# Optimization experiments

Hardware: AMD Instinct MI355X
Metric: run time of the kernel (lower is better)

Reference implementation:

```python
import jax, jax.numpy as jnp
import numpy as np

H = 4            # attention heads
D_SUB = 32       # per-head hidden dim
D_HID = H * D_SUB
B = 100          # graphs in batch
N_PER = 5000     # nodes per graph
N = B * N_PER
DEG = 16         # avg degree
E = N * DEG
K_PER = 2500     # ceil(0.5 * N_PER), pooling_rate=0.5


def setup_inputs() -> dict:
    key = jax.random.key(0)
    k0, k1, k2, k3 = jax.random.split(key, 4)
    x = jax.random.normal(k0, (N, D_HID), jnp.float32)
    sub_xs = jax.random.normal(k1, (H, N, D_SUB), jnp.float32)
    # edges strictly within each graph (contiguous node blocks per graph)
    rng = np.random.default_rng(0)
    src = rng.integers(0, N_PER, size=(B, N_PER * DEG))
    dst = rng.integers(0, N_PER, size=(B, N_PER * DEG))
    off = (np.arange(B) * N_PER)[:, None]
    edge_index = jnp.asarray(
        np.stack([(src + off).reshape(-1), (dst + off).reshape(-1)]), jnp.int32)
    batch = jnp.repeat(jnp.arange(B, dtype=jnp.int32), N_PER)
    att_W = jax.random.normal(k2, (H, D_SUB, 1), jnp.float32) * 0.1
    att_b = jnp.zeros((H, 1), jnp.float32)
    score_W = jax.random.normal(k3, (1, 1), jnp.float32)
    score_b = jnp.zeros((1,), jnp.float32)
    return {"x": x, "sub_xs": sub_xs, "att_W": att_W, "att_b": att_b,
            "score_W": score_W, "score_b": score_b,
            "edge_index": edge_index, "batch": batch}


def _gcn_prop(h, row, col, dis):
    # PyG GCNConv propagation with self-loops: D^{-1/2}(A+I)D^{-1/2} h
    norm = (dis[row] * dis[col])[:, None]                       # [E,1]
    agg = jax.ops.segment_sum(h[row] * norm, col, num_segments=N)
    return agg + h * (dis ** 2)[:, None]                        # self-loop term deg^-1


def reference(x, sub_xs, att_W, att_b, score_W, score_b, edge_index, batch):
    row, col = edge_index[0], edge_index[1]
    deg = 1.0 + jax.ops.segment_sum(jnp.ones((E,), x.dtype), col, num_segments=N)
    dis = deg ** -0.5
    # per-head GCNConv(sub_hidden, 1): [H,N,1]
    h = jnp.einsum('hnd,hdo->hno', sub_xs, att_W)
    agg = jax.vmap(lambda hh: _gcn_prop(hh, row, col, dis))(h) + att_b[:, None, :]
    # torch F.softmax with implicit dim=1 on [N,1] -> softmax over size-1 axis (all ones); faithful
    att = jax.nn.softmax(agg, axis=-1)                          # [H,N,1]
    pool = att.mean(axis=0)                                     # 'mean' att pooling -> [N,1]
    # pooling_score_layer = GCNConv(1,1)
    score = (_gcn_prop(pool @ score_W, row, col, dis) + score_b)[:, 0]  # [N]
    # batched topk: equal-size contiguous graphs -> static k per graph
    _, idx = jax.lax.top_k(score.reshape(B, N_PER), K_PER)      # sorted desc per graph
    perm = (idx + (jnp.arange(B) * N_PER)[:, None]).reshape(-1) # [B*K_PER]
    x_new = x[perm] * jnp.tanh(score[perm])[:, None]            # global att weighting
    batch_new = batch[perm]
    # filter_adj: keep edges with both endpoints selected, reindex to new ids
    n_idx = jnp.full((N,), -1, jnp.int32).at[perm].set(
        jnp.arange(B * K_PER, dtype=jnp.int32))
    r, c = n_idx[row], n_idx[col]
    keep = (r >= 0) & (c >= 0)
    pos = jnp.nonzero(keep, size=E, fill_value=0)[0]            # compacted, order-preserving
    valid = jnp.arange(E) < keep.sum()
    edge_new = jnp.stack([jnp.where(valid, r[pos], -1),
                          jnp.where(valid, c[pos], -1)])        # [2,E], -1 padded
    return x_new, edge_new, batch_new, perm
```

## Files before the change

### kernel.cpp

```cpp
#include <hip/hip_runtime.h>
#include <hip/hip_bf16.h>

constexpr int H      = 4;
constexpr int D_SUB  = 32;
constexpr int D_HID  = 128;
constexpr int B      = 100;
constexpr int N_PER  = 5000;
constexpr int N      = B * N_PER;
constexpr int DEG    = 16;
constexpr int E      = N * DEG;
constexpr int E_PER  = N_PER * DEG;
constexpr int K_PER  = 2500;
constexpr int NK     = B * K_PER;

constexpr int EPB    = 4096;
constexpr int EPT    = 16;
constexpr int NBLK_E = (E + EPB - 1) / EPB;

constexpr int SUBR   = 625;
constexpr int LCAP   = 11640;

constexpr int M      = 8192;

constexpr unsigned long long FLG_A = 1ull << 62;
constexpr unsigned long long FLG_I = 2ull << 62;

__device__ __forceinline__ int swz8(int bid, int chunk) {
    return (bid & 7) * chunk + (bid >> 3);
}

__device__ __forceinline__ int ph(int i) { return i + (i >> 3); }

__global__ __launch_bounds__(1024) void k_count(const int* __restrict__ col,
                                                int* __restrict__ cnt2) {
    __shared__ int h[N_PER];
    int lb = swz8(blockIdx.x, 25);
    int g = lb >> 1, half = lb & 1;
    for (int i = threadIdx.x; i < N_PER; i += 1024) h[i] = 0;
    __syncthreads();
    int ebase = g * E_PER + half * (E_PER / 2);
    int nbase = g * N_PER;
    const int4* c4 = (const int4*)(col + ebase);
    for (int i = threadIdx.x; i < E_PER / 2 / 4; i += 1024) {
        int4 v = c4[i];
        atomicAdd(&h[v.x - nbase], 1);
        atomicAdd(&h[v.y - nbase], 1);
        atomicAdd(&h[v.z - nbase], 1);
        atomicAdd(&h[v.w - nbase], 1);
    }
    __syncthreads();
    int* dst = cnt2 + half * N + nbase;
    for (int i = threadIdx.x; i < N_PER; i += 1024) dst[i] = h[i];
}

__global__ void k_dis(const int* __restrict__ cnt2, int* __restrict__ cnt,
                      float* __restrict__ dis) {
    int v = blockIdx.x * blockDim.x + threadIdx.x;
    if (v < N) {
        int c = cnt2[v] + cnt2[N + v];
        cnt[v] = c;
        float d = (float)(1 + c);
        dis[v] = __fdiv_rn(1.0f, __fsqrt_rn(d));
    }
}

__global__ __launch_bounds__(1024) void k_score_fused(const int* __restrict__ row,
                                                      const int* __restrict__ col,
                                                      const int* __restrict__ cnt,
                                                      const float* __restrict__ dis,
                                                      const float* __restrict__ scW,
                                                      const float* __restrict__ scB,
                                                      float* __restrict__ score) {
    __shared__ float dis_l[N_PER];
    __shared__ int   wsum[16];
    __shared__ int   offs_l[SUBR];
    __shared__ int   curs_l[SUBR];
    __shared__ int   list[LCAP];
    int lb = swz8(blockIdx.x, 100);
    int g = lb >> 3, q = lb & 7;
    int t = threadIdx.x;
    int nbase = g * N_PER;
    int ebase = g * E_PER;
    int lo = q * SUBR;

    const float4* d4 = (const float4*)(dis + nbase);
    for (int j4 = t; j4 < N_PER / 4; j4 += 1024) {
        float4 dv4 = d4[j4];
        int j = 4 * j4;
        dis_l[j]     = dv4.x;
        dis_l[j + 1] = dv4.y;
        dis_l[j + 2] = dv4.z;
        dis_l[j + 3] = dv4.w;
    }

    int v = (t < SUBR) ? cnt[nbase + lo + t] : 0;
    int lane = t & 63, wid = t >> 6;
    int x = v;
#pragma unroll
    for (int s = 1; s < 64; s <<= 1) {
        int o = __shfl_up(x, s, 64);
        if (lane >= s) x += o;
    }
    if (lane == 63) wsum[wid] = x;
    __syncthreads();
    if (wid == 0) {
        int ws = (lane < 16) ? wsum[lane] : 0;
#pragma unroll
        for (int s = 1; s < 16; s <<= 1) {
            int o = __shfl_up(ws, s, 64);
            if (lane >= s) ws += o;
        }
        if (lane < 16) wsum[lane] = ws;
    }
    __syncthreads();
    int incl = x + (wid > 0 ? wsum[wid - 1] : 0);
    if (t < SUBR) { offs_l[t] = incl - v + t; curs_l[t] = 0; }
    __syncthreads();

    const int4* c4 = (const int4*)(col + ebase);
    const int4* r4 = (const int4*)(row + ebase);
    for (int i4 = t; i4 < E_PER / 4; i4 += 1024) {
        int4 cv = c4[i4];
        int4 rv = r4[i4];
        int i0 = 4 * i4;
#pragma unroll
        for (int m = 0; m < 4; m++) {
            int cl = ((m == 0) ? cv.x : (m == 1) ? cv.y : (m == 2) ? cv.z : cv.w) - nbase;
            int rl = ((m == 0) ? rv.x : (m == 1) ? rv.y : (m == 2) ? rv.z : rv.w) - nbase;
            unsigned d = (unsigned)(cl - lo);
            if (d < (unsigned)SUBR) {
                int i = i0 + m;
                int slot = atomicAdd(&curs_l[d], 1);
                int pos = offs_l[d] + slot;
                if (pos < LCAP) list[pos] = (i << 13) | rl;
            }
        }
    }
    __syncthreads();

    if (t < SUBR) {
        int base = offs_l[t];
        int k = v;
        if (base + k > LCAP) k = 0;
        for (int i = 1; i < k; i++) {
            int key = list[base + i];
            int j = i - 1;
            while (j >= 0 && list[base + j] > key) { list[base + j + 1] = list[base + j]; j--; }
            list[base + j + 1] = key;
        }
        float w = scW[0];
        float dv = dis_l[lo + t];
        float s = 0.0f;
        for (int i = 0; i < k; i++) {
            int rl = list[base + i] & 8191;
            s = __fadd_rn(s, __fmul_rn(w, __fmul_rn(dis_l[rl], dv)));
        }
        s = __fadd_rn(s, __fmul_rn(w, __fmul_rn(dv, dv)));
        s = __fadd_rn(s, scB[0]);
        score[nbase + lo + t] = s;
    }
}

__global__ __launch_bounds__(1024) void k_topk(const float* __restrict__ score,
                                               float* __restrict__ out_batch,
                                               float* __restrict__ out_perm,
                                               int* __restrict__ perm_i,
                                               int* __restrict__ n_idx) {
    __shared__ unsigned long long keys[M + (M >> 3)];
    int b = blockIdx.x, t = threadIdx.x;
    int base = 8 * t;

    unsigned long long v[8];
    if (t < 625) {
        const float4* s4 = (const float4*)(score + b * N_PER + base);
        float4 f0 = s4[0], f1 = s4[1];
        float fs[8] = {f0.x, f0.y, f0.z, f0.w, f1.x, f1.y, f1.z, f1.w};
#pragma unroll
        for (int m = 0; m < 8; m++) {
            unsigned u = __float_as_uint(fs[m]);
            unsigned asc = u ^ ((u & 0x80000000u) ? 0xFFFFFFFFu : 0x80000000u);
            v[m] = ((unsigned long long)(~asc) << 32) | (unsigned)(base + m);
        }
    } else {
#pragma unroll
        for (int m = 0; m < 8; m++) v[m] = ~0ull;
    }

#define CEV(x, y, up) { if ((v[x] > v[y]) == (up)) { unsigned long long tmp = v[x]; v[x] = v[y]; v[y] = tmp; } }
    CEV(0, 1, true)  CEV(2, 3, false) CEV(4, 5, true)  CEV(6, 7, false)
    CEV(0, 2, true)  CEV(1, 3, true)  CEV(4, 6, false) CEV(5, 7, false)
    CEV(0, 1, true)  CEV(2, 3, true)  CEV(4, 5, false) CEV(6, 7, false)
    {
        bool u8 = ((t & 1) == 0);
        CEV(0, 4, u8) CEV(1, 5, u8) CEV(2, 6, u8) CEV(3, 7, u8)
        CEV(0, 2, u8) CEV(1, 3, u8) CEV(4, 6, u8) CEV(5, 7, u8)
        CEV(0, 1, u8) CEV(2, 3, u8) CEV(4, 5, u8) CEV(6, 7, u8)
    }
#pragma unroll
    for (int m = 0; m < 8; m++) keys[ph(base + m)] = v[m];
    __syncthreads();

    for (int k = 16; k <= M; k <<= 1) {
        bool last = (k == M);
        for (int j = k >> 1; j >= 8; j >>= 1) {
            int np = (last && j < (M >> 1)) ? (M >> 2) : (M >> 1);
            for (int p = t; p < np; p += 1024) {
                int i = ((p & ~(j - 1)) << 1) | (p & (j - 1));
                int ip = i | j;
                bool up = ((i & k) == 0);
                unsigned long long a = keys[ph(i)];
                unsigned long long c = keys[ph(ip)];
                if ((a > c) == up) { keys[ph(i)] = c; keys[ph(ip)] = a; }
            }
            __syncthreads();
        }
        int nb = last ? 512 : 1024;
        if (t < nb) {
            bool up = ((base & k) == 0);
            unsigned long long w[8];
#pragma unroll
            for (int m = 0; m < 8; m++) w[m] = keys[ph(base + m)];
#define CEW(x, y) { if ((w[x] > w[y]) == up) { unsigned long long tmp = w[x]; w[x] = w[y]; w[y] = tmp; } }
            CEW(0, 4) CEW(1, 5) CEW(2, 6) CEW(3, 7)
            CEW(0, 2) CEW(1, 3) CEW(4, 6) CEW(5, 7)
            CEW(0, 1) CEW(2, 3) CEW(4, 5) CEW(6, 7)
#pragma unroll
            for (int m = 0; m < 8; m++) keys[ph(base + m)] = w[m];
        }
        __syncthreads();
    }

    for (int r = t; r < K_PER; r += 1024) {
        unsigned long long key = keys[ph(r)];
        int idx = (int)(key & 0xFFFFFFFFull);
        int gl = b * N_PER + idx;
        int ni = b * K_PER + r;
        perm_i[ni] = gl;
        n_idx[gl] = ni;
        out_perm[ni] = (float)gl;
        out_batch[ni] = (float)b;
    }
}

__global__ void k_xnew(const float4* __restrict__ x4, const float* __restrict__ score,
                       const int* __restrict__ perm_i, float4* __restrict__ out4) {
    int tid = blockIdx.x * blockDim.x + threadIdx.x;
    if (tid >= NK * (D_HID / 4)) return;
    int i = tid >> 5;
    int c = tid & 31;
    int g = perm_i[i];
    float ts = tanhf(score[g]);
    float4 v = x4[(long)g * 32 + c];
    v.x *= ts; v.y *= ts; v.z *= ts; v.w *= ts;
    out4[tid] = v;
}

__global__ void k_prefill(float4* __restrict__ oe0, float4* __restrict__ oe1,
                          int4* __restrict__ n_idx4,
                          unsigned long long* __restrict__ status) {
    int i = blockIdx.x * blockDim.x + threadIdx.x;
    int stride = gridDim.x * blockDim.x;
    float4 m1 = make_float4(-1.0f, -1.0f, -1.0f, -1.0f);
    for (int j = i; j < E / 4; j += stride) { oe0[j] = m1; oe1[j] = m1; }
    int4 mi = make_int4(-1, -1, -1, -1);
    for (int j = i; j < N / 4; j += stride) n_idx4[j] = mi;
    for (int j = i; j < NBLK_E; j += stride) status[j] = 0ull;
}

__global__ __launch_bounds__(256) void k_compact(const int* __restrict__ row,
                                                 const int* __restrict__ col,
                                                 const int* __restrict__ n_idx,
                                                 unsigned long long* __restrict__ status,
                                                 float* __restrict__ oe0,
                                                 float* __restrict__ oe1) {
    __shared__ int sh[256];
    __shared__ int excl_sh;
    int blk = blockIdx.x, t = threadIdx.x;
    int base = blk * EPB + t * EPT;
    int rr[EPT], cc[EPT];
    int cnt = 0;
    if (blk < NBLK_E - 1) {
#pragma unroll
        for (int i4 = 0; i4 < 4; i4++) {
            int4 rv = ((const int4*)(row + base))[i4];
            int4 cv = ((const int4*)(col + base))[i4];
            rr[4 * i4 + 0] = n_idx[rv.x];  cc[4 * i4 + 0] = n_idx[cv.x];
            rr[4 * i4 + 1] = n_idx[rv.y];  cc[4 * i4 + 1] = n_idx[cv.y];
            rr[4 * i4 + 2] = n_idx[rv.z];  cc[4 * i4 + 2] = n_idx[cv.z];
            rr[4 * i4 + 3] = n_idx[rv.w];  cc[4 * i4 + 3] = n_idx[cv.w];
        }
#pragma unroll
        for (int i = 0; i < EPT; i++)
            if (rr[i] >= 0 && cc[i] >= 0) cnt++;
    } else {
#pragma unroll
        for (int i = 0; i < EPT; i++) {
            int e = base + i;
            int rv = -1, cv = -1;
            if (e < E) { rv = n_idx[row[e]]; cv = n_idx[col[e]]; }
            rr[i] = rv; cc[i] = cv;
            if (rv >= 0 && cv >= 0) cnt++;
        }
    }
    sh[t] = cnt;
    __syncthreads();
    for (int s = 1; s < 256; s <<= 1) {
        int a = (t >= s) ? sh[t - s] : 0;
        __syncthreads();
        sh[t] += a;
        __syncthreads();
    }
    int incl = sh[t];
    int agg  = sh[255];
    if (t == 0) {
        if (blk == 0) {
            atomicExch(&status[0], FLG_I | (unsigned long long)(unsigned)agg);
            excl_sh = 0;
        } else {
            atomicExch(&status[blk], FLG_A | (unsigned long long)(unsigned)agg);
            unsigned long long ex = 0;
            for (int i = blk - 1; i >= 0; i--) {
                unsigned long long sv;
                do { sv = atomicAdd(&status[i], 0ull); } while (sv == 0ull);
                ex += (sv & 0xFFFFFFFFull);
                if (sv & FLG_I) break;
            }
            atomicExch(&status[blk], FLG_I | (ex + (unsigned long long)(unsigned)agg));
            excl_sh = (int)ex;
        }
    }
    __syncthreads();
    int pos = excl_sh + incl - cnt;
#pragma unroll
    for (int i = 0; i < EPT; i++) {
        if (rr[i] >= 0 && cc[i] >= 0) {
            oe0[pos] = (float)rr[i];
            oe1[pos] = (float)cc[i];
            pos++;
        }
    }
}

extern "C" void kernel_launch(void* const* d_in, const int* in_sizes, int n_in,
                              void* d_out, int out_size, void* d_ws, size_t ws_size,
                              hipStream_t stream) {
    const float* x   = (const float*)d_in[0];
    const float* scW = (const float*)d_in[4];
    const float* scB = (const float*)d_in[5];
    const int*   edge = (const int*)d_in[6];
    const int*   row = edge;
    const int*   col = edge + E;

    unsigned long long* status = (unsigned long long*)d_ws;
    int*   ws_i    = (int*)(status + NBLK_E);
    int*   cnt2    = ws_i;
    int*   deg_cnt = ws_i + 2 * N;
    float* dis     = (float*)(ws_i + 3 * N);
    float* score   = (float*)(ws_i + 4 * N);
    int*   n_idx   = ws_i + 5 * N;
    int*   perm_i  = ws_i + 6 * N;

    float* out_x     = (float*)d_out;
    float* oe0       = out_x + (size_t)NK * D_HID;
    float* oe1       = oe0 + E;
    float* out_batch = oe1 + E;
    float* out_perm  = out_batch + NK;

    k_prefill<<<2048, 256, 0, stream>>>((float4*)oe0, (float4*)oe1, (int4*)n_idx, status);
    k_count<<<200, 1024, 0, stream>>>(col, cnt2);
    k_dis<<<(N + 255) / 256, 256, 0, stream>>>(cnt2, deg_cnt, dis);
    k_score_fused<<<800, 1024, 0, stream>>>(row, col, deg_cnt, dis, scW, scB, score);
    k_topk<<<B, 1024, 0, stream>>>(score, out_batch, out_perm, perm_i, n_idx);
    k_xnew<<<(NK * (D_HID / 4) + 255) / 256, 256, 0, stream>>>((const float4*)x, score, perm_i,
                                                               (float4*)out_x);
    k_compact<<<NBLK_E, 256, 0, stream>>>(row, col, n_idx, status, oe0, oe1);
}
```

Before: 258.0 us.

## Replace per-node insertion sort with wave-ordered stable counting scatter in score kernel

The score kernel now builds a per-wave, per-destination histogram in shared memory, prefix-scans it into per-wave starting offsets, and scatters source ids in edge order using ballot-aggregated atomics. Because each wave's slice is already ordered, the per-node lists come out in edge order without the serial insertion sort, so the summation order stays the same. It also drops the separate degree-count buffer and shrinks list entries to 16-bit. In exchange it adds a second pass over col, a histogram with packed 16-bit counters, and a per-iteration ballot loop that may serialise when many lanes hit distinct destinations.

```diff
diff --git a/kernel.cpp b/kernel.cpp
--- a/kernel.cpp
+++ b/kernel.cpp
@@ -18,7 +18,8 @@
 constexpr int NBLK_E = (E + EPB - 1) / EPB;
 
 constexpr int SUBR   = 625;
-constexpr int LCAP   = 11640;
+constexpr int LCAP_E = 12640;
+constexpr int WEDG   = E_PER / 16;
 
 constexpr int M      = 8192;
 
@@ -53,12 +54,10 @@
     for (int i = threadIdx.x; i < N_PER; i += 1024) dst[i] = h[i];
 }
 
-__global__ void k_dis(const int* __restrict__ cnt2, int* __restrict__ cnt,
-                      float* __restrict__ dis) {
+__global__ void k_dis(const int* __restrict__ cnt2, float* __restrict__ dis) {
     int v = blockIdx.x * blockDim.x + threadIdx.x;
     if (v < N) {
         int c = cnt2[v] + cnt2[N + v];
-        cnt[v] = c;
         float d = (float)(1 + c);
         dis[v] = __fdiv_rn(1.0f, __fsqrt_rn(d));
     }
@@ -66,19 +65,20 @@
 
 __global__ __launch_bounds__(1024) void k_score_fused(const int* __restrict__ row,
                                                       const int* __restrict__ col,
-                                                      const int* __restrict__ cnt,
                                                       const float* __restrict__ dis,
                                                       const float* __restrict__ scW,
                                                       const float* __restrict__ scB,
                                                       float* __restrict__ score) {
     __shared__ float dis_l[N_PER];
-    __shared__ int   wsum[16];
-    __shared__ int   offs_l[SUBR];
-    __shared__ int   curs_l[SUBR];
-    __shared__ int   list[LCAP];
+    __shared__ unsigned hist[8 * SUBR];
+    __shared__ int offs_l[SUBR];
+    __shared__ int kd_l[SUBR];
+    __shared__ int wsum[16];
+    __shared__ unsigned short list[LCAP_E];
     int lb = swz8(blockIdx.x, 100);
     int g = lb >> 3, q = lb & 7;
     int t = threadIdx.x;
+    int w = t >> 6, lane = t & 63;
     int nbase = g * N_PER;
     int ebase = g * E_PER;
     int lo = q * SUBR;
@@ -87,23 +87,45 @@
     for (int j4 = t; j4 < N_PER / 4; j4 += 1024) {
         float4 dv4 = d4[j4];
         int j = 4 * j4;
-        dis_l[j]     = dv4.x;
-        dis_l[j + 1] = dv4.y;
-        dis_l[j + 2] = dv4.z;
-        dis_l[j + 3] = dv4.w;
-    }
-
-    int v = (t < SUBR) ? cnt[nbase + lo + t] : 0;
-    int lane = t & 63, wid = t >> 6;
-    int x = v;
+        dis_l[j] = dv4.x; dis_l[j + 1] = dv4.y; dis_l[j + 2] = dv4.z; dis_l[j + 3] = dv4.w;
+    }
+    for (int i = t; i < 8 * SUBR; i += 1024) hist[i] = 0;
+    __syncthreads();
+
+    {
+        const int4* c4 = (const int4*)(col + ebase + w * WEDG);
+        unsigned inc = 1u << ((w & 1) * 16);
+        unsigned* hrow = hist + (w >> 1) * SUBR;
+        for (int i4 = lane; i4 < WEDG / 4; i4 += 64) {
+            int4 cv = c4[i4];
+#pragma unroll
+            for (int m = 0; m < 4; m++) {
+                int dl = ((m == 0) ? cv.x : (m == 1) ? cv.y : (m == 2) ? cv.z : cv.w) - nbase - lo;
+                if ((unsigned)dl < (unsigned)SUBR) atomicAdd(&hrow[dl], inc);
+            }
+        }
+    }
+    __syncthreads();
+
+    unsigned c8[8];
+    int kd = 0;
+    if (t < SUBR) {
+#pragma unroll
+        for (int j = 0; j < 8; j++) {
+            c8[j] = hist[j * SUBR + t];
+            kd += (int)(c8[j] & 0xFFFFu) + (int)(c8[j] >> 16);
+        }
+        kd_l[t] = kd;
+    }
+    int x = kd;
 #pragma unroll
     for (int s = 1; s < 64; s <<= 1) {
         int o = __shfl_up(x, s, 64);
         if (lane >= s) x += o;
     }
-    if (lane == 63) wsum[wid] = x;
-    __syncthreads();
-    if (wid == 0) {
+    if (lane == 63) wsum[w] = x;
+    __syncthreads();
+    if (w == 0) {
         int ws = (lane < 16) ? wsum[lane] : 0;
 #pragma unroll
         for (int s = 1; s < 16; s <<= 1) {
@@ -113,26 +135,52 @@
         if (lane < 16) wsum[lane] = ws;
     }
     __syncthreads();
-    int incl = x + (wid > 0 ? wsum[wid - 1] : 0);
-    if (t < SUBR) { offs_l[t] = incl - v + t; curs_l[t] = 0; }
-    __syncthreads();
-
-    const int4* c4 = (const int4*)(col + ebase);
-    const int4* r4 = (const int4*)(row + ebase);
-    for (int i4 = t; i4 < E_PER / 4; i4 += 1024) {
-        int4 cv = c4[i4];
-        int4 rv = r4[i4];
-        int i0 = 4 * i4;
-#pragma unroll
-        for (int m = 0; m < 4; m++) {
-            int cl = ((m == 0) ? cv.x : (m == 1) ? cv.y : (m == 2) ? cv.z : cv.w) - nbase;
-            int rl = ((m == 0) ? rv.x : (m == 1) ? rv.y : (m == 2) ? rv.z : rv.w) - nbase;
-            unsigned d = (unsigned)(cl - lo);
-            if (d < (unsigned)SUBR) {
-                int i = i0 + m;
-                int slot = atomicAdd(&curs_l[d], 1);
-                int pos = offs_l[d] + slot;
-                if (pos < LCAP) list[pos] = (i << 13) | rl;
+    if (t < SUBR) {
+        int incl = x + (w > 0 ? wsum[w - 1] : 0);
+        int base = incl - kd + 2 * t;
+        offs_l[t] = base;
+        unsigned run = (unsigned)base;
+#pragma unroll
+        for (int j = 0; j < 8; j++) {
+            unsigned lo16 = run & 0xFFFFu;  run += (c8[j] & 0xFFFFu);
+            unsigned hi16 = run & 0xFFFFu;  run += (c8[j] >> 16);
+            hist[j * SUBR + t] = lo16 | (hi16 << 16);
+        }
+    }
+    __syncthreads();
+
+    {
+        const int* cw = col + ebase + w * WEDG;
+        const int* rw = row + ebase + w * WEDG;
+        unsigned wsh = (unsigned)((w & 1) * 16);
+        unsigned* hrow = hist + (w >> 1) * SUBR;
+        for (int b = 0; b < (WEDG + 63) / 64; b++) {
+            int idx = b * 64 + lane;
+            bool m = false; int dl = 0, rl = 0;
+            if (idx < WEDG) {
+                dl = cw[idx] - nbase - lo;
+                m = ((unsigned)dl < (unsigned)SUBR);
+                if (m) rl = rw[idx] - nbase;
+            }
+            unsigned long long mm = __ballot(m);
+            while (mm) {
+                int leader = (int)__ffsll((long long)mm) - 1;
+                int dl0 = __shfl(dl, leader);
+                unsigned long long same = __ballot(m && dl == dl0);
+                int cntd = __popcll(same);
+                int base = 0;
+                if (lane == leader) {
+                    unsigned old = atomicAdd(&hrow[dl0], (unsigned)cntd << wsh);
+                    base = (int)((old >> wsh) & 0xFFFFu);
+                }
+                base = __shfl(base, leader);
+                if (m && dl == dl0) {
+                    int myr = __popcll(same & ((1ull << lane) - 1ull));
+                    int pos = base + myr;
+                    if (pos < LCAP_E) list[pos] = (unsigned short)rl;
+                    m = false;
+                }
+                mm &= ~same;
             }
         }
     }
@@ -140,22 +188,16 @@
 
     if (t < SUBR) {
         int base = offs_l[t];
-        int k = v;
-        if (base + k > LCAP) k = 0;
-        for (int i = 1; i < k; i++) {
-            int key = list[base + i];
-            int j = i - 1;
-            while (j >= 0 && list[base + j] > key) { list[base + j + 1] = list[base + j]; j--; }
-            list[base + j + 1] = key;
-        }
-        float w = scW[0];
+        int k = kd_l[t];
+        if (base + k > LCAP_E) k = 0;
+        float w0 = scW[0];
         float dv = dis_l[lo + t];
         float s = 0.0f;
         for (int i = 0; i < k; i++) {
-            int rl = list[base + i] & 8191;
-            s = __fadd_rn(s, __fmul_rn(w, __fmul_rn(dis_l[rl], dv)));
-        }
-        s = __fadd_rn(s, __fmul_rn(w, __fmul_rn(dv, dv)));
+            int rl = list[base + i];
+            s = __fadd_rn(s, __fmul_rn(w0, __fmul_rn(dis_l[rl], dv)));
+        }
+        s = __fadd_rn(s, __fmul_rn(w0, __fmul_rn(dv, dv)));
         s = __fadd_rn(s, scB[0]);
         score[nbase + lo + t] = s;
     }
@@ -354,11 +396,10 @@
     unsigned long long* status = (unsigned long long*)d_ws;
     int*   ws_i    = (int*)(status + NBLK_E);
     int*   cnt2    = ws_i;
-    int*   deg_cnt = ws_i + 2 * N;
-    float* dis     = (float*)(ws_i + 3 * N);
-    float* score   = (float*)(ws_i + 4 * N);
-    int*   n_idx   = ws_i + 5 * N;
-    int*   perm_i  = ws_i + 6 * N;
+    float* dis     = (float*)(ws_i + 2 * N);
+    float* score   = (float*)(ws_i + 3 * N);
+    int*   n_idx   = ws_i + 4 * N;
+    int*   perm_i  = ws_i + 5 * N;
 
     float* out_x     = (float*)d_out;
     float* oe0       = out_x + (size_t)NK * D_HID;
@@ -368,8 +409,8 @@
 
     k_prefill<<<2048, 256, 0, stream>>>((float4*)oe0, (float4*)oe1, (int4*)n_idx, status);
     k_count<<<200, 1024, 0, stream>>>(col, cnt2);
-    k_dis<<<(N + 255) / 256, 256, 0, stream>>>(cnt2, deg_cnt, dis);
-    k_score_fused<<<800, 1024, 0, stream>>>(row, col, deg_cnt, dis, scW, scB, score);
+    k_dis<<<(N + 255) / 256, 256, 0, stream>>>(cnt2, dis);
+    k_score_fused<<<800, 1024, 0, stream>>>(row, col, dis, scW, scB, score);
     k_topk<<<B, 1024, 0, stream>>>(score, out_batch, out_perm, perm_i, n_idx);
     k_xnew<<<(NK * (D_HID / 4) + 255) / 256, 256, 0, stream>>>((const float4*)x, score, perm_i,
                                                                (float4*)out_x);
```

After: 629.0 us. 144% more time.
